# Performance work log

Measured on AMD Instinct MI355X. Metric: run time of the kernel, lower is better.

## Reference

```python
import jax, jax.numpy as jnp
import numpy as np

BS, T, S_LEN = 128, 256, 40
NV, NS = 2048, 300
VH, SH = 512, 512
L_CROSS, N_LOC, N_FEAT = 512, 128, 1024


def _linear_params(key, out_d, in_d):
    k1, k2 = jax.random.split(key)
    lim = 1.0 / np.sqrt(in_d)
    W = jax.random.uniform(k1, (out_d, in_d), jnp.float32, -lim, lim)
    b = jax.random.uniform(k2, (out_d,), jnp.float32, -lim, lim)
    return W, b


def setup_inputs() -> dict:
    key = jax.random.key(0)
    ks = jax.random.split(key, 12)
    gv = jax.random.normal(ks[0], (BS, T, NV), jnp.float32)
    sen = jax.random.normal(ks[1], (BS, S_LEN, NS), jnp.float32)
    visual_fea = jax.random.normal(ks[2], (BS, T, 2 * VH), jnp.float32)
    sen_fea = jax.random.normal(ks[3], (BS, 2 * SH), jnp.float32)
    loc = jax.random.uniform(ks[4], (BS, 2), jnp.float32)  # normalized start/end in [0,1)
    v_len = jax.random.randint(ks[5], (BS,), 1, T + 1)
    video_mask = (jnp.arange(T)[None, :] < v_len[:, None]).astype(jnp.int32)
    s_len = jax.random.randint(ks[6], (BS,), 1, S_LEN + 1)
    sen_mask = (jnp.arange(S_LEN)[None, :] < s_len[:, None]).astype(jnp.int32)
    W1, b1 = _linear_params(ks[7], L_CROSS, 2 * VH)
    W2, b2 = _linear_params(ks[8], L_CROSS, 2 * SH)
    W3, b3 = _linear_params(ks[9], N_LOC, 2)
    n_cat = 2 * (VH + SH) + L_CROSS + N_LOC
    W4, b4 = _linear_params(ks[10], N_FEAT, n_cat)
    return dict(step=1, gv=gv, sen=sen, visual_fea=visual_fea, sen_fea=sen_fea,
                loc=loc, sen_mask=sen_mask, video_mask=video_mask,
                W1=W1, b1=b1, W2=W2, b2=b2, W3=W3, b3=b3, W4=W4, b4=b4)


def _pool_and_head(visual_fea, sen_fea, loc, video_mask,
                   W1, b1, W2, b2, W3, b3, W4, b4):
    dt = visual_fea.dtype
    n_frame = visual_fea.shape[1]
    v_len = video_mask.sum(1)  # [B] int
    valid = (jnp.arange(n_frame)[None, :] < v_len[:, None]).astype(dt)  # [B,T]
    # global mean over valid frames
    gv_fea = (visual_fea * valid[:, :, None]).sum(1) / v_len[:, None].astype(dt)
    # local mean over [start, end] with start/end = floor(loc * (len-1)) (torch int() trunc, loc>=0)
    idx = jnp.floor(loc * (v_len[:, None] - 1).astype(loc.dtype)).astype(jnp.int32)
    s, e = idx[:, 0], idx[:, 1]
    csum = jnp.cumsum(visual_fea, axis=1)
    csum = jnp.concatenate([jnp.zeros_like(csum[:, :1]), csum], axis=1)  # [B,T+1,D]
    seg_sum = (jnp.take_along_axis(csum, (e + 1)[:, None, None], axis=1)
               - jnp.take_along_axis(csum, s[:, None, None], axis=1))[:, 0, :]
    cnt = jnp.maximum(e + 1 - s, 1).astype(dt)
    lv_fea = jnp.where((s <= e)[:, None], seg_sum / cnt[:, None], jnp.zeros((), dt))
    # fused head
    vs = jax.nn.relu((lv_fea @ W1.T + b1) * (sen_fea @ W2.T + b2))
    loc_fea = jax.nn.relu(loc @ W3.T + b3)
    out = jnp.concatenate([sen_fea, gv_fea, vs, loc_fea], axis=1)
    feature = jax.nn.relu(out @ W4.T + b4)
    return feature


def reference(step, gv, sen, visual_fea, sen_fea, loc, sen_mask, video_mask,
              W1, b1, W2, b2, W3, b3, W4, b4):
    # step != 0 hot path: GRU encodes (step==0 one-time branch) are skipped;
    # visual_fea / sen_fea are carried over from the step-0 call, as in the original.
    assert step != 0, 'reference covers the recurrent hot path (step > 0)'
    feature = _pool_and_head(visual_fea, sen_fea, loc, video_mask,
                             W1, b1, W2, b2, W3, b3, W4, b4)
    return visual_fea, sen_fea, feature
```

## Files before the change

### kernel.cpp

```cpp
#include <hip/hip_runtime.h>

#define BS 128
#define T 256
#define D 1024
#define NCAT 2688
#define NFEAT 1024

typedef short bf16x8 __attribute__((ext_vector_type(8)));
typedef float f32x4 __attribute__((ext_vector_type(4)));
typedef unsigned short u16;
typedef u16 u16x4 __attribute__((ext_vector_type(4)));

__device__ __forceinline__ u16 f2bf(float f) {
    unsigned int u = __float_as_uint(f);
    u += 0x7fffu + ((u >> 16) & 1u);
    return (u16)(u >> 16);
}

__global__ __launch_bounds__(256, 4)
void ka(const float* __restrict__ vf, float* __restrict__ out0,
        const int* __restrict__ vmask, const float* __restrict__ loc,
        const float* __restrict__ sen_fea,
        const float* __restrict__ W1, const float* __restrict__ W2,
        const float* __restrict__ W3, const float* __restrict__ W4,
        const float* __restrict__ b3,
        u16* __restrict__ W1b, u16* __restrict__ W2b, u16* __restrict__ W4b,
        float* __restrict__ pgv, float* __restrict__ pseg,
        u16* __restrict__ cat, float* __restrict__ out1) {
    int blk = blockIdx.x, tid = threadIdx.x;

    if (blk >= 4736) {
        int b = blk - 4736;
        int d0 = tid * 4;
        f32x4 sf = *(const f32x4*)(sen_fea + b * D + d0);
        *(f32x4*)(out1 + b * D + d0) = sf;
        u16x4 sb;
        sb[0] = f2bf(sf[0]); sb[1] = f2bf(sf[1]); sb[2] = f2bf(sf[2]); sb[3] = f2bf(sf[3]);
        *(u16x4*)(cat + b * NCAT + d0) = sb;
        if (tid < 128) {
            float v = loc[2 * b] * W3[2 * tid] + loc[2 * b + 1] * W3[2 * tid + 1] + b3[tid];
            cat[b * NCAT + 2560 + tid] = f2bf(fmaxf(v, 0.f));
        }
        return;
    }

    if (blk >= 1024) {
        int i = (blk - 1024) * 256 + tid;
        const float* src; u16* dst;
        if (i < 131072)      { src = W1 + 4 * i;            dst = W1b + 4 * i; }
        else if (i < 262144) { src = W2 + 4 * (i - 131072); dst = W2b + 4 * (i - 131072); }
        else                 { src = W4 + 4 * (i - 262144); dst = W4b + 4 * (i - 262144); }
        f32x4 v = *(const f32x4*)src;
        u16x4 o;
        o[0] = f2bf(v[0]); o[1] = f2bf(v[1]); o[2] = f2bf(v[2]); o[3] = f2bf(v[3]);
        *(u16x4*)dst = o;
        return;
    }

    int b = blk >> 3, tc = blk & 7;
    __shared__ int red[256];
    __shared__ int sse[3];
    red[tid] = vmask[b * T + tid];
    __syncthreads();
    for (int off = 128; off > 0; off >>= 1) {
        if (tid < off) red[tid] += red[tid + off];
        __syncthreads();
    }
    if (tid == 0) {
        int vl = red[0];
        float sc = (float)(vl - 1);
        sse[0] = vl;
        sse[1] = (int)floorf(loc[2 * b] * sc);
        sse[2] = (int)floorf(loc[2 * b + 1] * sc);
    }
    __syncthreads();
    int vl = sse[0], s = sse[1], e = sse[2];

    int t0 = tc * 32;
    int d0 = tid * 4;
    f32x4 g  = {0.f, 0.f, 0.f, 0.f};
    f32x4 sg = {0.f, 0.f, 0.f, 0.f};
    const float* src = vf   + ((size_t)(b * T + t0)) * D + d0;
    float*       dst = out0 + ((size_t)(b * T + t0)) * D + d0;
    for (int i = 0; i < 32; ++i) {
        f32x4 v = *(const f32x4*)src;
        __builtin_nontemporal_store(v, (f32x4*)dst);
        int t = t0 + i;
        if (t < vl) g += v;
        if (t >= s && t <= e) sg += v;
        src += D; dst += D;
    }
    int o = (b * 8 + tc) * D + d0;
    *(f32x4*)(pgv  + o) = g;
    *(f32x4*)(pseg + o) = sg;
}

__global__ void k2p(const float* __restrict__ loc, const int* __restrict__ vmask,
                    const float* __restrict__ pgv, const float* __restrict__ pseg,
                    u16* __restrict__ lv_bf, u16* __restrict__ cat) {
    int b = blockIdx.x, tid = threadIdx.x;
    __shared__ int red[256];
    __shared__ int sse[3];
    red[tid] = vmask[b * T + tid];
    __syncthreads();
    for (int off = 128; off > 0; off >>= 1) {
        if (tid < off) red[tid] += red[tid + off];
        __syncthreads();
    }
    if (tid == 0) {
        int vl = red[0];
        float sc = (float)(vl - 1);
        sse[0] = vl;
        sse[1] = (int)floorf(loc[2 * b] * sc);
        sse[2] = (int)floorf(loc[2 * b + 1] * sc);
    }
    __syncthreads();
    int vl = sse[0], s = sse[1], e = sse[2];
    float inv_vl = 1.0f / (float)vl;
    int cnt = e + 1 - s; if (cnt < 1) cnt = 1;
    float inv_cnt = 1.0f / (float)cnt;
    bool valid = (s <= e);

    for (int d = tid; d < D; d += 256) {
        float gs = 0.f, ss = 0.f;
#pragma unroll
        for (int c = 0; c < 8; ++c) {
            gs += pgv [(b * 8 + c) * D + d];
            ss += pseg[(b * 8 + c) * D + d];
        }
        cat[b * NCAT + 1024 + d] = f2bf(gs * inv_vl);
        lv_bf[b * D + d] = f2bf(valid ? ss * inv_cnt : 0.f);
    }
}

__global__ void kBC(const u16* __restrict__ lv, const u16* __restrict__ cat_ro,
                    const u16* __restrict__ W1b, const float* __restrict__ b1,
                    const u16* __restrict__ W2b, const float* __restrict__ b2,
                    const u16* __restrict__ W4b, u16* __restrict__ cat,
                    float* __restrict__ part) {
    int blk = blockIdx.x, tid = threadIdx.x;

    if (blk < 128) {
        __shared__ float qs[2][4][64];
        int mt = blk >> 4, ntg = blk & 15;
        int sub = tid >> 7, chain = (tid >> 6) & 1, lane = tid & 63;
        int m0 = mt * 16, n0 = ntg * 32 + sub * 16;
        int row = lane & 15, kg = lane >> 4;

        const u16* pa = chain ? (cat_ro + (m0 + row) * NCAT + kg * 8)
                              : (lv     + (m0 + row) * D    + kg * 8);
        const u16* pb = (chain ? W2b : W1b) + (n0 + row) * D + kg * 8;

        f32x4 acc = {0.f, 0.f, 0.f, 0.f};
        for (int k = 0; k < 1024; k += 32)
            acc = __builtin_amdgcn_mfma_f32_16x16x32_bf16(*(const bf16x8*)(pa + k),
                                                          *(const bf16x8*)(pb + k),
                                                          acc, 0, 0, 0);
        int col = lane & 15, rbase = (lane >> 4) * 4;
        float bb = (chain ? b2 : b1)[n0 + col];
        if (chain) {
#pragma unroll
            for (int r = 0; r < 4; ++r) qs[sub][r][lane] = acc[r] + bb;
        }
        __syncthreads();
        if (!chain) {
#pragma unroll
            for (int r = 0; r < 4; ++r) {
                float p = acc[r] + bb;
                cat[(m0 + rbase + r) * NCAT + 2048 + n0 + col] =
                    f2bf(fmaxf(p * qs[sub][r][lane], 0.f));
            }
        }
        return;
    }

    __shared__ float qsf[3][4][64];
    int bi = blk - 128;
    int mt = bi >> 6, nt = bi & 63;
    int wid = tid >> 6, lane = tid & 63;
    int m0 = mt * 16, n0 = nt * 16;
    int row = lane & 15, kg = lane >> 4;

    const u16* pa = cat_ro + (m0 + row) * NCAT + kg * 8;
    const u16* pb = W4b    + (n0 + row) * NCAT + kg * 8;

    f32x4 acc = {0.f, 0.f, 0.f, 0.f};
    for (int k = 0; k < 544; k += 32) {
        int ccol = wid * 544 + k;
        int acol = ccol + (ccol >= 2048 ? 512 : 0);
        acc = __builtin_amdgcn_mfma_f32_16x16x32_bf16(*(const bf16x8*)(pa + acol),
                                                      *(const bf16x8*)(pb + acol),
                                                      acc, 0, 0, 0);
    }
    int lane64 = lane;
    if (wid) {
#pragma unroll
        for (int r = 0; r < 4; ++r) qsf[wid - 1][r][lane64] = acc[r];
    }
    __syncthreads();
    if (wid == 0) {
#pragma unroll
        for (int r = 0; r < 4; ++r)
            part[bi * 256 + r * 64 + lane64] =
                acc[r] + qsf[0][r][lane64] + qsf[1][r][lane64] + qsf[2][r][lane64];
    }
}

__global__ void k4b(const u16* __restrict__ cat, const u16* __restrict__ W4b,
                    const float* __restrict__ b4, const float* __restrict__ part,
                    float* __restrict__ out2) {
    int blk = blockIdx.x, tid = threadIdx.x;
    __shared__ float qs[4][64];

    int mt = blk >> 6, nt = blk & 63;
    int wid = tid >> 6, lane = tid & 63;
    int m0 = mt * 16, n0 = nt * 16;
    int row = lane & 15, kg = lane >> 4;

    const u16* pa = cat + (m0 + row) * NCAT + 2048 + wid * 256 + kg * 8;
    const u16* pb = W4b + (n0 + row) * NCAT + 2048 + wid * 256 + kg * 8;

    f32x4 acc = {0.f, 0.f, 0.f, 0.f};
    for (int k = 0; k < 256; k += 32)
        acc = __builtin_amdgcn_mfma_f32_16x16x32_bf16(*(const bf16x8*)(pa + k),
                                                      *(const bf16x8*)(pb + k),
                                                      acc, 0, 0, 0);
    int col = lane & 15, rbase = (lane >> 4) * 4;
    if (wid == 1) {
#pragma unroll
        for (int r = 0; r < 4; ++r) qs[r][lane] = acc[r];
    }
    __syncthreads();
    if (wid == 0) {
        float bb = b4[n0 + col];
#pragma unroll
        for (int r = 0; r < 4; ++r) {
            float v = acc[r] + qs[r][lane] + part[blk * 256 + r * 64 + lane] + bb;
            out2[(m0 + rbase + r) * NFEAT + n0 + col] = fmaxf(v, 0.f);
        }
    }
}

extern "C" void kernel_launch(void* const* d_in, const int* in_sizes, int n_in,
                              void* d_out, int out_size, void* d_ws, size_t ws_size,
                              hipStream_t stream) {
    (void)in_sizes; (void)n_in; (void)out_size; (void)ws_size;
    const float* vf      = (const float*)d_in[3];
    const float* sen_fea = (const float*)d_in[4];
    const float* loc     = (const float*)d_in[5];
    const int*   vmask   = (const int*)d_in[7];
    const float* W1 = (const float*)d_in[8];
    const float* b1 = (const float*)d_in[9];
    const float* W2 = (const float*)d_in[10];
    const float* b2 = (const float*)d_in[11];
    const float* W3 = (const float*)d_in[12];
    const float* b3 = (const float*)d_in[13];
    const float* W4 = (const float*)d_in[14];
    const float* b4 = (const float*)d_in[15];

    float* out0 = (float*)d_out;
    float* out1 = out0 + (size_t)BS * T * D;
    float* out2 = out1 + (size_t)BS * D;

    char* w = (char*)d_ws;
    float* pgv  = (float*)(w);
    float* pseg = (float*)(w + (4 << 20));
    u16*   cat  = (u16*)  (w + (8 << 20));
    u16*   W1b  = (u16*)  (w + (9 << 20));
    u16*   W2b  = (u16*)  (w + (10 << 20));
    u16*   W4b  = (u16*)  (w + (11 << 20));
    float* part = (float*)(w + (17 << 20));
    u16*   lv   = (u16*)  (w + (18 << 20));

    ka<<<4864, 256, 0, stream>>>(vf, out0, vmask, loc, sen_fea,
                                 W1, W2, W3, W4, b3,
                                 W1b, W2b, W4b, pgv, pseg, cat, out1);
    k2p<<<128, 256, 0, stream>>>(loc, vmask, pgv, pseg, lv, cat);
    kBC<<<640, 256, 0, stream>>>(lv, cat, W1b, b1, W2b, b2, W4b, cat, part);
    k4b<<<512, 128, 0, stream>>>(cat, W4b, b4, part, out2);
}
```

Baseline: 74.51 us.

## Fold pooling reduction into first kernel and drop partial-sum pass

```diff
diff --git a/kernel.cpp b/kernel.cpp
--- a/kernel.cpp
+++ b/kernel.cpp
@@ -25,12 +25,84 @@
         const float* __restrict__ W3, const float* __restrict__ W4,
         const float* __restrict__ b3,
         u16* __restrict__ W1b, u16* __restrict__ W2b, u16* __restrict__ W4b,
-        float* __restrict__ pgv, float* __restrict__ pseg,
-        u16* __restrict__ cat, float* __restrict__ out1) {
+        u16* __restrict__ cat, u16* __restrict__ lv, float* __restrict__ out1) {
     int blk = blockIdx.x, tid = threadIdx.x;
 
-    if (blk >= 4736) {
-        int b = blk - 4736;
+    if (blk < 128) {
+        int b = blk;
+        __shared__ int red[256];
+        __shared__ int sse[3];
+        red[tid] = vmask[b * T + tid];
+        __syncthreads();
+        for (int off = 128; off > 0; off >>= 1) {
+            if (tid < off) red[tid] += red[tid + off];
+            __syncthreads();
+        }
+        if (tid == 0) {
+            int vl = red[0];
+            float sc = (float)(vl - 1);
+            sse[0] = vl;
+            sse[1] = (int)floorf(loc[2 * b] * sc);
+            sse[2] = (int)floorf(loc[2 * b + 1] * sc);
+        }
+        __syncthreads();
+        int vl = sse[0], s = sse[1], e = sse[2];
+
+        int d0 = tid * 4;
+        f32x4 g  = {0.f, 0.f, 0.f, 0.f};
+        f32x4 sg = {0.f, 0.f, 0.f, 0.f};
+        const float* src = vf + (size_t)b * T * D + d0;
+#pragma unroll 8
+        for (int t = 0; t < 256; ++t) {
+            f32x4 v = *(const f32x4*)src;
+            if (t < vl) g += v;
+            if (t >= s && t <= e) sg += v;
+            src += D;
+        }
+        float inv_vl = 1.0f / (float)vl;
+        int cnt = e + 1 - s; if (cnt < 1) cnt = 1;
+        float inv_cnt = 1.0f / (float)cnt;
+        bool valid = (s <= e);
+        u16x4 og, ol;
+#pragma unroll
+        for (int j = 0; j < 4; ++j) {
+            og[j] = f2bf(g[j] * inv_vl);
+            ol[j] = f2bf(valid ? sg[j] * inv_cnt : 0.f);
+        }
+        *(u16x4*)(cat + b * NCAT + 1024 + d0) = og;
+        *(u16x4*)(lv + b * D + d0) = ol;
+        return;
+    }
+
+    if (blk < 1152) {
+        int ci = blk - 128;
+        int b = ci >> 3, tc = ci & 7;
+        int d0 = tid * 4;
+        const float* src = vf   + ((size_t)(b * T + tc * 32)) * D + d0;
+        float*       dst = out0 + ((size_t)(b * T + tc * 32)) * D + d0;
+        for (int i = 0; i < 32; ++i) {
+            f32x4 v = *(const f32x4*)src;
+            __builtin_nontemporal_store(v, (f32x4*)dst);
+            src += D; dst += D;
+        }
+        return;
+    }
+
+    if (blk < 4864) {
+        int i = (blk - 1152) * 256 + tid;
+        const float* src; u16* dst;
+        if (i < 131072)      { src = W1 + 4 * i;            dst = W1b + 4 * i; }
+        else if (i < 262144) { src = W2 + 4 * (i - 131072); dst = W2b + 4 * (i - 131072); }
+        else                 { src = W4 + 4 * (i - 262144); dst = W4b + 4 * (i - 262144); }
+        f32x4 v = *(const f32x4*)src;
+        u16x4 o;
+        o[0] = f2bf(v[0]); o[1] = f2bf(v[1]); o[2] = f2bf(v[2]); o[3] = f2bf(v[3]);
+        *(u16x4*)dst = o;
+        return;
+    }
+
+    {
+        int b = blk - 4864;
         int d0 = tid * 4;
         f32x4 sf = *(const f32x4*)(sen_fea + b * D + d0);
         *(f32x4*)(out1 + b * D + d0) = sf;
@@ -41,95 +113,6 @@
             float v = loc[2 * b] * W3[2 * tid] + loc[2 * b + 1] * W3[2 * tid + 1] + b3[tid];
             cat[b * NCAT + 2560 + tid] = f2bf(fmaxf(v, 0.f));
         }
-        return;
-    }
-
-    if (blk >= 1024) {
-        int i = (blk - 1024) * 256 + tid;
-        const float* src; u16* dst;
-        if (i < 131072)      { src = W1 + 4 * i;            dst = W1b + 4 * i; }
-        else if (i < 262144) { src = W2 + 4 * (i - 131072); dst = W2b + 4 * (i - 131072); }
-        else                 { src = W4 + 4 * (i - 262144); dst = W4b + 4 * (i - 262144); }
-        f32x4 v = *(const f32x4*)src;
-        u16x4 o;
-        o[0] = f2bf(v[0]); o[1] = f2bf(v[1]); o[2] = f2bf(v[2]); o[3] = f2bf(v[3]);
-        *(u16x4*)dst = o;
-        return;
-    }
-
-    int b = blk >> 3, tc = blk & 7;
-    __shared__ int red[256];
-    __shared__ int sse[3];
-    red[tid] = vmask[b * T + tid];
-    __syncthreads();
-    for (int off = 128; off > 0; off >>= 1) {
-        if (tid < off) red[tid] += red[tid + off];
-        __syncthreads();
-    }
-    if (tid == 0) {
-        int vl = red[0];
-        float sc = (float)(vl - 1);
-        sse[0] = vl;
-        sse[1] = (int)floorf(loc[2 * b] * sc);
-        sse[2] = (int)floorf(loc[2 * b + 1] * sc);
-    }
-    __syncthreads();
-    int vl = sse[0], s = sse[1], e = sse[2];
-
-    int t0 = tc * 32;
-    int d0 = tid * 4;
-    f32x4 g  = {0.f, 0.f, 0.f, 0.f};
-    f32x4 sg = {0.f, 0.f, 0.f, 0.f};
-    const float* src = vf   + ((size_t)(b * T + t0)) * D + d0;
-    float*       dst = out0 + ((size_t)(b * T + t0)) * D + d0;
-    for (int i = 0; i < 32; ++i) {
-        f32x4 v = *(const f32x4*)src;
-        __builtin_nontemporal_store(v, (f32x4*)dst);
-        int t = t0 + i;
-        if (t < vl) g += v;
-        if (t >= s && t <= e) sg += v;
-        src += D; dst += D;
-    }
-    int o = (b * 8 + tc) * D + d0;
-    *(f32x4*)(pgv  + o) = g;
-    *(f32x4*)(pseg + o) = sg;
-}
-
-__global__ void k2p(const float* __restrict__ loc, const int* __restrict__ vmask,
-                    const float* __restrict__ pgv, const float* __restrict__ pseg,
-                    u16* __restrict__ lv_bf, u16* __restrict__ cat) {
-    int b = blockIdx.x, tid = threadIdx.x;
-    __shared__ int red[256];
-    __shared__ int sse[3];
-    red[tid] = vmask[b * T + tid];
-    __syncthreads();
-    for (int off = 128; off > 0; off >>= 1) {
-        if (tid < off) red[tid] += red[tid + off];
-        __syncthreads();
-    }
-    if (tid == 0) {
-        int vl = red[0];
-        float sc = (float)(vl - 1);
-        sse[0] = vl;
-        sse[1] = (int)floorf(loc[2 * b] * sc);
-        sse[2] = (int)floorf(loc[2 * b + 1] * sc);
-    }
-    __syncthreads();
-    int vl = sse[0], s = sse[1], e = sse[2];
-    float inv_vl = 1.0f / (float)vl;
-    int cnt = e + 1 - s; if (cnt < 1) cnt = 1;
-    float inv_cnt = 1.0f / (float)cnt;
-    bool valid = (s <= e);
-
-    for (int d = tid; d < D; d += 256) {
-        float gs = 0.f, ss = 0.f;
-#pragma unroll
-        for (int c = 0; c < 8; ++c) {
-            gs += pgv [(b * 8 + c) * D + d];
-            ss += pseg[(b * 8 + c) * D + d];
-        }
-        cat[b * NCAT + 1024 + d] = f2bf(gs * inv_vl);
-        lv_bf[b * D + d] = f2bf(valid ? ss * inv_cnt : 0.f);
     }
 }
 
@@ -185,24 +168,27 @@
     const u16* pb = W4b    + (n0 + row) * NCAT + kg * 8;
 
     f32x4 acc = {0.f, 0.f, 0.f, 0.f};
-    for (int k = 0; k < 544; k += 32) {
-        int ccol = wid * 544 + k;
-        int acol = ccol + (ccol >= 2048 ? 512 : 0);
-        acc = __builtin_amdgcn_mfma_f32_16x16x32_bf16(*(const bf16x8*)(pa + acol),
-                                                      *(const bf16x8*)(pb + acol),
+    int kb = wid * 512;
+    for (int k = 0; k < 512; k += 32)
+        acc = __builtin_amdgcn_mfma_f32_16x16x32_bf16(*(const bf16x8*)(pa + kb + k),
+                                                      *(const bf16x8*)(pb + kb + k),
                                                       acc, 0, 0, 0);
-    }
-    int lane64 = lane;
+    if (wid == 0) {
+        for (int k = 2560; k < 2688; k += 32)
+            acc = __builtin_amdgcn_mfma_f32_16x16x32_bf16(*(const bf16x8*)(pa + k),
+                                                          *(const bf16x8*)(pb + k),
+                                                          acc, 0, 0, 0);
+    }
     if (wid) {
 #pragma unroll
-        for (int r = 0; r < 4; ++r) qsf[wid - 1][r][lane64] = acc[r];
+        for (int r = 0; r < 4; ++r) qsf[wid - 1][r][lane] = acc[r];
     }
     __syncthreads();
     if (wid == 0) {
 #pragma unroll
         for (int r = 0; r < 4; ++r)
-            part[bi * 256 + r * 64 + lane64] =
-                acc[r] + qsf[0][r][lane64] + qsf[1][r][lane64] + qsf[2][r][lane64];
+            part[bi * 256 + r * 64 + lane] =
+                acc[r] + qsf[0][r][lane] + qsf[1][r][lane] + qsf[2][r][lane];
     }
 }
 
@@ -263,19 +249,16 @@
     float* out2 = out1 + (size_t)BS * D;
 
     char* w = (char*)d_ws;
-    float* pgv  = (float*)(w);
-    float* pseg = (float*)(w + (4 << 20));
-    u16*   cat  = (u16*)  (w + (8 << 20));
-    u16*   W1b  = (u16*)  (w + (9 << 20));
-    u16*   W2b  = (u16*)  (w + (10 << 20));
-    u16*   W4b  = (u16*)  (w + (11 << 20));
-    float* part = (float*)(w + (17 << 20));
-    u16*   lv   = (u16*)  (w + (18 << 20));
-
-    ka<<<4864, 256, 0, stream>>>(vf, out0, vmask, loc, sen_fea,
+    u16*   cat  = (u16*)  (w);
+    u16*   W1b  = (u16*)  (w + (1 << 20));
+    u16*   W2b  = (u16*)  (w + (2 << 20));
+    u16*   W4b  = (u16*)  (w + (3 << 20));
+    float* part = (float*)(w + (9 << 20));
+    u16*   lv   = (u16*)  (w + (10 << 20));
+
+    ka<<<4992, 256, 0, stream>>>(vf, out0, vmask, loc, sen_fea,
                                  W1, W2, W3, W4, b3,
-                                 W1b, W2b, W4b, pgv, pseg, cat, out1);
-    k2p<<<128, 256, 0, stream>>>(loc, vmask, pgv, pseg, lv, cat);
+                                 W1b, W2b, W4b, cat, lv, out1);
     kBC<<<640, 256, 0, stream>>>(lv, cat, W1b, b1, W2b, b2, W4b, cat, part);
     k4b<<<512, 128, 0, stream>>>(cat, W4b, b4, part, out2);
 }
```

After: 88.30 us. 18.5% more time.
